# Performance work log

Hardware: AMD Instinct MI355X
Metric: run time of the kernel (lower is better)

Reference implementation:

```python
import jax, jax.numpy as jnp
import numpy as np

# Model dims
C = 16          # in_channels / d_model
D_INNER = 64    # expand * C, expand = 64 // C = 4
HEADDIM = 4
NHEADS = D_INNER // HEADDIM   # 16
D_STATE = 64
D_CONV = 4
CONV_DIM = D_INNER + 2 * D_STATE        # 192 (x, B, C streams)
D_IN_PROJ = 2 * D_INNER + 2 * D_STATE + NHEADS  # 272 (z, xBC, dt)
# Input volume
BSZ, DD, HH, WW = 8, 32, 16, 16
L = DD * HH * WW  # 8192, multiple of 256 -> exact adaptive max pool
POOL = 256


def setup_inputs():
    key = jax.random.key(0)
    ks = jax.random.split(key, 10)
    x = jax.random.normal(ks[0], (BSZ, C, DD, HH, WW), jnp.float32)
    # 3 independent Mamba2 blocks -> stack params with leading dim 3
    Win = jax.random.normal(ks[1], (3, D_IN_PROJ, C), jnp.float32) / np.sqrt(C).astype(np.float32)
    conv_w = jax.random.normal(ks[2], (3, CONV_DIM, D_CONV), jnp.float32) / np.sqrt(D_CONV).astype(np.float32)
    conv_b = jax.random.normal(ks[3], (3, CONV_DIM), jnp.float32) * 0.1
    dt_bias = jax.random.normal(ks[4], (3, NHEADS), jnp.float32) * 0.5
    A_log = jnp.log(jax.random.uniform(ks[5], (3, NHEADS), jnp.float32, minval=1.0, maxval=16.0))
    Dp = jax.random.normal(ks[6], (3, NHEADS), jnp.float32) * 0.5 + 1.0
    norm_w = jnp.ones((3, D_INNER), jnp.float32)
    Wout = jax.random.normal(ks[7], (3, C, D_INNER), jnp.float32) / np.sqrt(D_INNER).astype(np.float32)
    gamma = jnp.ones((3, C), jnp.float32)
    beta = jnp.zeros((3, C), jnp.float32)
    lin_w = jax.random.normal(ks[8], (3, 1, C), jnp.float32) / np.sqrt(C).astype(np.float32)
    lin_b = jnp.zeros((3, 1), jnp.float32)
    return dict(x=x, Win=Win, conv_w=conv_w, conv_b=conv_b, dt_bias=dt_bias,
                A_log=A_log, Dp=Dp, norm_w=norm_w, Wout=Wout,
                gamma=gamma, beta=beta, lin_w=lin_w, lin_b=lin_b)


def _mamba2(u, Win, conv_w, conv_b, dt_bias, A_log, Dp, norm_w, Wout):
    """Mamba2 block: u (B, L, C) -> (B, L, C). ngroups=1, rmsnorm gated."""
    B, Lx, _ = u.shape
    zxbcdt = jnp.einsum('blc,pc->blp', u, Win)  # (B, L, 272)
    z = zxbcdt[..., :D_INNER]
    xBC = zxbcdt[..., D_INNER:D_INNER + CONV_DIM]
    dt = jax.nn.softplus(zxbcdt[..., D_INNER + CONV_DIM:] + dt_bias)  # (B, L, H)
    # causal depthwise conv over time
    conv = jax.lax.conv_general_dilated(
        jnp.transpose(xBC, (0, 2, 1)), conv_w[:, None, :], (1,),
        [(D_CONV - 1, 0)], feature_group_count=CONV_DIM)
    xBC = jax.nn.silu(jnp.transpose(conv, (0, 2, 1)) + conv_b)
    xh = xBC[..., :D_INNER].reshape(B, Lx, NHEADS, HEADDIM)
    Bm = xBC[..., D_INNER:D_INNER + D_STATE]   # (B, L, N)
    Cm = xBC[..., D_INNER + D_STATE:]          # (B, L, N)
    A = -jnp.exp(A_log)                        # (H,)
    dA = jnp.exp(dt * A)                       # (B, L, H)
    dtx = dt[..., None] * xh                   # (B, L, H, P)

    def step(S, inp):
        dA_t, dtx_t, B_t, C_t = inp
        S = S * dA_t[:, :, None, None] + dtx_t[..., None] * B_t[:, None, None, :]
        y_t = jnp.einsum('bhpn,bn->bhp', S, C_t)
        return S, y_t

    S0 = jnp.zeros((B, NHEADS, HEADDIM, D_STATE), u.dtype)
    xs = (jnp.moveaxis(dA, 1, 0), jnp.moveaxis(dtx, 1, 0),
          jnp.moveaxis(Bm, 1, 0), jnp.moveaxis(Cm, 1, 0))
    _, ys = jax.lax.scan(step, S0, xs)                       # (L, B, H, P)
    y = jnp.moveaxis(ys, 0, 1) + Dp[None, None, :, None] * xh
    y = y.reshape(B, Lx, D_INNER) * jax.nn.silu(z)           # gate first
    y = y * jax.lax.rsqrt(jnp.mean(y * y, -1, keepdims=True) + 1e-5) * norm_w
    return jnp.einsum('bld,cd->blc', y, Wout)


def _proj_pool(y, gamma, beta, lw, lb):
    """ReLU -> BatchNorm1d (batch stats) -> Linear(C,1) -> AdaptiveMaxPool1d(256)."""
    B, Lx, _ = y.shape
    v = jax.nn.relu(y.reshape(-1, C))
    mu = jnp.mean(v, 0)
    var = jnp.mean((v - mu) ** 2, 0)
    v = (v - mu) * jax.lax.rsqrt(var + 1e-5) * gamma + beta
    s = (v @ lw.T + lb).reshape(B, Lx)
    return jnp.max(s.reshape(B, POOL, Lx // POOL), -1)  # (B, 256)


def reference(x, Win, conv_w, conv_b, dt_bias, A_log, Dp, norm_w, Wout,
              gamma, beta, lin_w, lin_b):
    B, Cc, Dd, Hh, Ww = x.shape
    Lx = Dd * Hh * Ww
    fD = jnp.transpose(x.reshape(B, Cc, Lx), (0, 2, 1))
    fH = jnp.transpose(jnp.transpose(x, (0, 1, 3, 4, 2)).reshape(B, Cc, Lx), (0, 2, 1))
    fW = jnp.transpose(jnp.transpose(x, (0, 1, 4, 2, 3)).reshape(B, Cc, Lx), (0, 2, 1))
    seqs = jnp.stack([fD, fH, fW], 0)  # (3, B, L, C)
    ys = jax.vmap(_mamba2)(seqs, Win, conv_w, conv_b, dt_bias, A_log, Dp, norm_w, Wout)
    pooled = jax.vmap(_proj_pool)(ys, gamma, beta, lin_w, lin_b)  # (3, B, 256)
    return jnp.concatenate([pooled[0], pooled[1], pooled[2]], -1)[:, None, :]  # (B,1,768)
```

## Files before the change

### kernel.cpp

```cpp
#include <hip/hip_runtime.h>
#include <math.h>

#define CONVD 192
#define NC 128
#define PW 32
#define LOG2E 1.4426950408889634f
#define LN2f  0.69314718055994531f

#define OFF_DST   0u
#define OFF_CHA   4194304u
#define OFF_YS    4210688u
#define OFF_PART  5259264u
#define OFF_TILE  5267456u
#define PD        19947520u

#define TG  0
#define TC  4096
#define TCS 8192
#define TDT 12288
#define TCT 13312

#define XSW(m, t)   ((m) * 64 + (((((t) >> 2) ^ ((m) & 15)) & 15) << 2) + ((t) & 3))
#define XSW4(m, tq) ((m) * 64 + ((((tq) ^ ((m) & 15)) & 15) << 2))

typedef float f32x2 __attribute__((ext_vector_type(2)));

__device__ __forceinline__ f32x2 pk_fma(f32x2 a, f32x2 b, f32x2 c) {
    f32x2 d;
    asm("v_pk_fma_f32 %0, %1, %2, %3" : "=v"(d) : "v"(a), "v"(b), "v"(c));
    return d;
}
__device__ __forceinline__ f32x2 pk_fma_alo(f32x2 a, f32x2 b, f32x2 c) {
    f32x2 d;
    asm("v_pk_fma_f32 %0, %1, %2, %3 op_sel_hi:[0,1,1]" : "=v"(d) : "v"(a), "v"(b), "v"(c));
    return d;
}
__device__ __forceinline__ f32x2 pk_fma_ahi(f32x2 a, f32x2 b, f32x2 c) {
    f32x2 d;
    asm("v_pk_fma_f32 %0, %1, %2, %3 op_sel:[1,0,0]" : "=v"(d) : "v"(a), "v"(b), "v"(c));
    return d;
}
__device__ __forceinline__ f32x2 pk_fma_blo(f32x2 a, f32x2 b, f32x2 c) {
    f32x2 d;
    asm("v_pk_fma_f32 %0, %1, %2, %3 op_sel_hi:[1,0,1]" : "=v"(d) : "v"(a), "v"(b), "v"(c));
    return d;
}
__device__ __forceinline__ f32x2 pk_fma_bhi(f32x2 a, f32x2 b, f32x2 c) {
    f32x2 d;
    asm("v_pk_fma_f32 %0, %1, %2, %3 op_sel:[0,1,0]" : "=v"(d) : "v"(a), "v"(b), "v"(c));
    return d;
}
__device__ __forceinline__ f32x2 lo2(float4 v) { f32x2 r; r.x = v.x; r.y = v.y; return r; }
__device__ __forceinline__ f32x2 hi2(float4 v) { f32x2 r; r.x = v.z; r.y = v.w; return r; }

__device__ __forceinline__ float fast_silu(float x) {
    float e = __builtin_amdgcn_exp2f(-x * LOG2E);
    return x * __builtin_amdgcn_rcpf(1.f + e);
}
__device__ __forceinline__ float fast_softplus(float x) {
    if (x > 20.f) return x;
    float e = __builtin_amdgcn_exp2f(x * LOG2E);
    return LN2f * __builtin_amdgcn_logf(1.f + e);
}

template<int NT, int STRIDE>
__device__ __forceinline__ void stage_u(
    const float* __restrict__ x, float* u_s, int b, int l0, int dir, int tid)
{
    for (int i = tid; i < 67 * 16; i += NT) {
        int pos = i >> 4, c = i & 15;
        int l = l0 + pos - 3;
        float v = 0.f;
        if (l >= 0) {
            if (dir == 0) {
                v = x[(b * 16 + c) * 8192 + l];
            } else if (dir == 1) {
                int h = l >> 9, w = (l >> 5) & 15, d = l & 31;
                v = x[(((b * 16 + c) * 32 + d) * 16 + h) * 16 + w];
            } else {
                int w = l >> 9, d = (l >> 4) & 31, h = l & 15;
                v = x[(((b * 16 + c) * 32 + d) * 16 + h) * 16 + w];
            }
        }
        u_s[pos * STRIDE + c] = v;
    }
}

__device__ __forceinline__ float pk_dot16(const f32x2* u2, const float* wp) {
    float4 w0 = *(const float4*)(wp);
    float4 w1 = *(const float4*)(wp + 4);
    float4 w2 = *(const float4*)(wp + 8);
    float4 w3 = *(const float4*)(wp + 12);
    f32x2 a = {0.f, 0.f};
    a = pk_fma(u2[0], lo2(w0), a);
    a = pk_fma(u2[1], hi2(w0), a);
    a = pk_fma(u2[2], lo2(w1), a);
    a = pk_fma(u2[3], hi2(w1), a);
    a = pk_fma(u2[4], lo2(w2), a);
    a = pk_fma(u2[5], hi2(w2), a);
    a = pk_fma(u2[6], lo2(w3), a);
    a = pk_fma(u2[7], hi2(w3), a);
    return a.x + a.y;
}

__global__ __launch_bounds__(512, 4) void k_delta(
    const float* __restrict__ x, const float* __restrict__ Win,
    const float* __restrict__ convw, const float* __restrict__ convb,
    const float* __restrict__ dtb, const float* __restrict__ A_log,
    float* __restrict__ ws, int dir0, int dslm)
{
    __shared__ float u_s[67 * 17];
    __shared__ float xh_c[4096];
    __shared__ float Bs[4096];
    __shared__ float Cc[4096];
    __shared__ float dts[16 * 65];
    __shared__ float wbuf[16 * 65];
    const int tid = threadIdx.x;
    const int ck = blockIdx.x;
    const int b = blockIdx.y;
    const int dir = dir0 + blockIdx.z;
    float* base = ws + (size_t)(dslm * blockIdx.z) * PD;
    float* Dst = base + OFF_DST;
    float* chA = base + OFF_CHA;
    float* tile = base + OFF_TILE + (size_t)(b * 128 + ck) * 14336;
    const int l0 = ck * 64;
    float* halo = wbuf;

    stage_u<512, 17>(x, u_s, b, l0, dir, tid);
    __syncthreads();

    const int lane = tid & 63;
    const int wv = __builtin_amdgcn_readfirstlane(tid >> 6);

    f32x2 u2[8];
    {
        const float* ur = &u_s[(lane + 3) * 17];
        #pragma unroll
        for (int k = 0; k < 8; k++) { u2[k].x = ur[2 * k]; u2[k].y = ur[2 * k + 1]; }
    }
    if (tid < 192) {
        f32x2 uh2[8];
        #pragma unroll
        for (int pos = 0; pos < 3; pos++) {
            const float* uhr = &u_s[pos * 17];
            #pragma unroll
            for (int k = 0; k < 8; k++) { uh2[k].x = uhr[2 * k]; uh2[k].y = uhr[2 * k + 1]; }
            halo[pos * 192 + tid] = pk_dot16(uh2, Win + (size_t)(dir * 272 + 64 + tid) * 16);
        }
    }
    __syncthreads();

    for (int i = 0; i < 26; i++) {
        const int g = wv * 26 + i;
        const int col = (g < 192) ? (64 + g) : (256 + (g - 192));
        float acc = pk_dot16(u2, Win + (size_t)(dir * 272 + col) * 16);
        if (col < 256) {
            const int ch = col - 64;
            float v1 = __shfl_up(acc, 1);
            float v2 = __shfl_up(acc, 2);
            float v3 = __shfl_up(acc, 3);
            float hh0 = halo[ch];
            float hh1 = halo[192 + ch];
            float hh2 = halo[384 + ch];
            float m1 = (lane >= 1) ? v1 : hh2;
            float m2 = (lane >= 2) ? v2 : ((lane == 0) ? hh1 : hh2);
            float m3 = (lane >= 3) ? v3 : ((lane == 0) ? hh0 : ((lane == 1) ? hh1 : hh2));
            const float* cwp = convw + (size_t)(dir * CONVD + ch) * 4;
            float conv = convb[dir * CONVD + ch]
                       + cwp[0] * m3 + cwp[1] * m2 + cwp[2] * m1 + cwp[3] * acc;
            float xv = fast_silu(conv);
            if (ch < 64)       xh_c[XSW(ch, lane)] = xv;
            else if (ch < 128) Bs[XSW(ch - 64, lane)] = xv;
            else               Cc[XSW(ch - 128, lane)] = xv;
        } else {
            const int h = col - 256;
            float dv = fast_softplus(acc + dtb[dir * 16 + h]);
            dts[h * 65 + lane] = dv;
            tile[TDT + h * 64 + lane] = dv;
        }
    }
    __syncthreads();

    for (int j4 = tid; j4 < 1024; j4 += 512)
        ((float4*)(tile + TC))[j4] = ((const float4*)Cc)[j4];
    for (int h = wv; h < 16; h += 8) {
        float A2 = -expf(A_log[dir * 16 + h]) * LOG2E;
        float dtv = dts[h * 65 + lane];
        float v = dtv * A2;
        #pragma unroll
        for (int off = 1; off < 64; off <<= 1) {
            float o = __shfl_up(v, off, 64);
            if (lane >= off) v += o;
        }
        float tot = __shfl(v, 63, 64);
        tile[TCT + h * 64 + lane] = v;
        wbuf[h * 65 + lane] = __builtin_amdgcn_exp2f(tot - v) * dtv;
        if (lane == 63) chA[(b * 16 + h) * 128 + ck] = __builtin_amdgcn_exp2f(tot);
    }
    __syncthreads();

    for (int j = tid; j < 4096; j += 512) {
        int hp = j >> 6, t = j & 63;
        xh_c[XSW(hp, t)] *= wbuf[(hp >> 2) * 65 + t];
    }
    __syncthreads();

    if (tid < 256) {
        const int hp4 = tid >> 4, n4 = tid & 15;
        f32x2 a2[4][4] = {};
        for (int tq = 0; tq < 16; tq++) {
            float4 xv[4], bv[4];
            #pragma unroll
            for (int i2 = 0; i2 < 4; i2++) {
                xv[i2] = *(const float4*)&xh_c[XSW4(4 * hp4 + i2, tq)];
                bv[i2] = *(const float4*)&Bs[XSW4(4 * n4 + i2, tq)];
            }
            #pragma unroll
            for (int i2 = 0; i2 < 4; i2++)
                #pragma unroll
                for (int j2 = 0; j2 < 4; j2++) {
                    a2[i2][j2] = pk_fma(lo2(xv[i2]), lo2(bv[j2]), a2[i2][j2]);
                    a2[i2][j2] = pk_fma(hi2(xv[i2]), hi2(bv[j2]), a2[i2][j2]);
                }
        }
        #pragma unroll
        for (int i2 = 0; i2 < 4; i2++) {
            int hp = 4 * hp4 + i2;
            int h = hp >> 2, p = hp & 3;
            *(float4*)(Dst + ((size_t)((b * 16 + h) * 128 + ck)) * 256 + p * 64 + 4 * n4) =
                make_float4(a2[i2][0].x + a2[i2][0].y, a2[i2][1].x + a2[i2][1].y,
                            a2[i2][2].x + a2[i2][2].y, a2[i2][3].x + a2[i2][3].y);
        }
    } else {
        const int tg2 = tid - 256;
        const int t4g = tg2 >> 4, x4g = tg2 & 15;
        f32x2 G2[4][2] = {};
        for (int n = 0; n < 64; n++) {
            float4 cr4 = *(const float4*)&Cc[XSW4(n, t4g)];
            float4 br4 = *(const float4*)&Bs[XSW4(n, x4g)];
            f32x2 c01 = lo2(cr4), c23 = hi2(cr4);
            f32x2 b01 = lo2(br4), b23 = hi2(br4);
            G2[0][0] = pk_fma_alo(c01, b01, G2[0][0]); G2[0][1] = pk_fma_alo(c01, b23, G2[0][1]);
            G2[1][0] = pk_fma_ahi(c01, b01, G2[1][0]); G2[1][1] = pk_fma_ahi(c01, b23, G2[1][1]);
            G2[2][0] = pk_fma_alo(c23, b01, G2[2][0]); G2[2][1] = pk_fma_alo(c23, b23, G2[2][1]);
            G2[3][0] = pk_fma_ahi(c23, b01, G2[3][0]); G2[3][1] = pk_fma_ahi(c23, b23, G2[3][1]);
        }
        float* gdst = tile + TG + (size_t)tg2 * 16;
        #pragma unroll
        for (int r = 0; r < 4; r++)
            *(float4*)(gdst + 4 * r) =
                make_float4(G2[r][0].x, G2[r][0].y, G2[r][1].x, G2[r][1].y);
    }
}

__global__ __launch_bounds__(64) void k_chunk_scan(
    float* __restrict__ ws, int dslm)
{
    float* base = ws + (size_t)(dslm * blockIdx.z) * PD;
    float* Dst = base + OFF_DST;
    const float* chA = base + OFF_CHA;
    const int bh = blockIdx.x >> 2;
    const int elem = (blockIdx.x & 3) * 64 + threadIdx.x;
    float S = 0.f;
    for (int k0 = 0; k0 < NC; k0 += 8) {
        float d[8], av[8];
        #pragma unroll
        for (int j = 0; j < 8; j++) {
            d[j] = Dst[((size_t)(bh * 128 + k0 + j)) * 256 + elem];
            av[j] = chA[bh * 128 + k0 + j];
        }
        #pragma unroll
        for (int j = 0; j < 8; j++) {
            Dst[((size_t)(bh * 128 + k0 + j)) * 256 + elem] = S;
            S = av[j] * S + d[j];
        }
    }
}

__global__ __launch_bounds__(256, 4) void k_cs(
    float* __restrict__ ws, int dslm)
{
    __shared__ float Ci[4096];
    __shared__ float SinT[64 * 66];
    float* base = ws + (size_t)(dslm * blockIdx.z) * PD;
    const float* Dst = base + OFF_DST;
    float* tile = base + OFF_TILE + (size_t)(blockIdx.y * 128 + blockIdx.x) * 14336;
    const int tid = threadIdx.x;
    const int b = blockIdx.y;
    const int ck = blockIdx.x;
    const int t4 = tid >> 4, x4 = tid & 15;

    for (int j4 = tid; j4 < 1024; j4 += 256)
        ((float4*)Ci)[j4] = ((const float4*)(tile + TC))[j4];
    for (int j = tid; j < 1024; j += 256) {
        int hp = j >> 4, n4 = (j & 15) << 2;
        int h = hp >> 2, p = hp & 3;
        float4 sv = *(const float4*)(Dst + ((size_t)((b * 16 + h) * 128 + ck)) * 256 + p * 64 + n4);
        SinT[(n4 + 0) * 66 + hp] = sv.x;
        SinT[(n4 + 1) * 66 + hp] = sv.y;
        SinT[(n4 + 2) * 66 + hp] = sv.z;
        SinT[(n4 + 3) * 66 + hp] = sv.w;
    }
    __syncthreads();

    f32x2 C2[4][2] = {};
    for (int n = 0; n < 64; n++) {
        float4 cr4 = *(const float4*)&Ci[XSW4(n, t4)];
        f32x2 c01 = lo2(cr4), c23 = hi2(cr4);
        f32x2 s01 = *(const f32x2*)&SinT[n * 66 + 4 * x4];
        f32x2 s23 = *(const f32x2*)&SinT[n * 66 + 4 * x4 + 2];
        C2[0][0] = pk_fma_alo(c01, s01, C2[0][0]); C2[0][1] = pk_fma_alo(c01, s23, C2[0][1]);
        C2[1][0] = pk_fma_ahi(c01, s01, C2[1][0]); C2[1][1] = pk_fma_ahi(c01, s23, C2[1][1]);
        C2[2][0] = pk_fma_alo(c23, s01, C2[2][0]); C2[2][1] = pk_fma_alo(c23, s23, C2[2][1]);
        C2[3][0] = pk_fma_ahi(c23, s01, C2[3][0]); C2[3][1] = pk_fma_ahi(c23, s23, C2[3][1]);
    }
    float* cdst = tile + TCS + (size_t)tid * 16;
    #pragma unroll
    for (int r = 0; r < 4; r++)
        *(float4*)(cdst + 4 * r) =
            make_float4(C2[r][0].x, C2[r][0].y, C2[r][1].x, C2[r][1].y);
}

__global__ __launch_bounds__(512, 6) void k_out_epi(
    const float* __restrict__ x, const float* __restrict__ Win,
    const float* __restrict__ convw, const float* __restrict__ convb,
    const float* __restrict__ Dp, const float* __restrict__ normw,
    const float* __restrict__ Wout, float* __restrict__ ws, int dir0, int dslm)
{
    __shared__ float uW[67 * 16];
    __shared__ float xh_c[4096];
    __shared__ float zc[4096];
    __shared__ float yv[4096];
    __shared__ float Dps[16];
    __shared__ float red[4][34];
    float* base = ws + (size_t)(dslm * blockIdx.z) * PD;
    float* ys       = base + OFF_YS;
    float* partials = base + OFF_PART;
    const float* tile = base + OFF_TILE + (size_t)(blockIdx.y * 128 + blockIdx.x) * 14336;
    const int dir = dir0 + blockIdx.z;
    const int tid = threadIdx.x;
    const int b = blockIdx.y;
    const int ck = blockIdx.x;
    const int l0 = ck * 64;
    const int tg = tid & 255;
    const int t4 = tg >> 4, x4 = tg & 15;
    const int grp = tid >> 8;
    const int lane = tid & 63;
    const int wv = __builtin_amdgcn_readfirstlane(tid >> 6);
    float* halo = yv;

    stage_u<512, 16>(x, uW, b, l0, dir, tid);
    if (tid < 16) Dps[tid] = Dp[dir * 16 + tid];
    __syncthreads();

    f32x2 u2[8];
    {
        const float* ur = &uW[(lane + 3) * 16];
        #pragma unroll
        for (int k = 0; k < 8; k++) { u2[k].x = ur[2 * k]; u2[k].y = ur[2 * k + 1]; }
    }
    if (tid < 64) {
        f32x2 uh2[8];
        #pragma unroll
        for (int pos = 0; pos < 3; pos++) {
            const float* uhr = &uW[pos * 16];
            #pragma unroll
            for (int k = 0; k < 8; k++) { uh2[k].x = uhr[2 * k]; uh2[k].y = uhr[2 * k + 1]; }
            halo[pos * 64 + tid] = pk_dot16(uh2, Win + (size_t)(dir * 272 + 64 + tid) * 16);
        }
    }
    __syncthreads();

    for (int i = 0; i < 8; i++) {
        const int col = wv * 8 + i;
        zc[XSW(col, lane)] = pk_dot16(u2, Win + (size_t)(dir * 272 + col) * 16);
    }
    for (int i = 0; i < 8; i++) {
        const int ch = wv * 8 + i;
        float acc = pk_dot16(u2, Win + (size_t)(dir * 272 + 64 + ch) * 16);
        float v1 = __shfl_up(acc, 1);
        float v2 = __shfl_up(acc, 2);
        float v3 = __shfl_up(acc, 3);
        float hh0 = halo[ch];
        float hh1 = halo[64 + ch];
        float hh2 = halo[128 + ch];
        float m1 = (lane >= 1) ? v1 : hh2;
        float m2 = (lane >= 2) ? v2 : ((lane == 0) ? hh1 : hh2);
        float m3 = (lane >= 3) ? v3 : ((lane == 0) ? hh0 : ((lane == 1) ? hh1 : hh2));
        const float* cwp = convw + (size_t)(dir * CONVD + ch) * 4;
        float conv = convb[dir * CONVD + ch]
                   + cwp[0] * m3 + cwp[1] * m2 + cwp[2] * m1 + cwp[3] * acc;
        xh_c[XSW(ch, lane)] = fast_silu(conv);
    }
    for (int j = tid; j < 1024; j += 512) {
        int c = j >> 6, d = j & 63;
        uW[c * 65 + d] = Wout[dir * 1024 + j] * normw[dir * 64 + d];
    }
    __syncthreads();

    float G_[4][4];
    {
        const float* gsrc = tile + TG + (size_t)tg * 16;
        #pragma unroll
        for (int r = 0; r < 4; r++) {
            float4 g4 = *(const float4*)(gsrc + 4 * r);
            G_[r][0] = g4.x; G_[r][1] = g4.y; G_[r][2] = g4.z; G_[r][3] = g4.w;
        }
    }

    const int tbase = 4 * t4;
    #pragma unroll 1
    for (int hh = 0; hh < 8; hh++) {
        const int h = 8 * grp + hh;
        const float* ctp = tile + TCT + h * 64;
        const float* dtp = tile + TDT + h * 64;
        float4 ctt4 = *(const float4*)(ctp + tbase);
        const float ctt[4] = {ctt4.x, ctt4.y, ctt4.z, ctt4.w};
        float4 cs4 = *(const float4*)(ctp + 4 * x4);
        float4 dt4 = *(const float4*)(dtp + 4 * x4);
        float4 xq[4];
        #pragma unroll
        for (int p = 0; p < 4; p++) {
            int m = 4 * h + p;
            xq[p] = *(const float4*)&xh_c[m * 64 + (((x4 ^ (m & 15)) & 15) << 2)];
        }
        f32x2 v2[2][4] = {};
        #pragma unroll
        for (int q = 0; q < 4; q++) {
            const int s = 4 * x4 + q;
            float csq = (q == 0) ? cs4.x : (q == 1) ? cs4.y : (q == 2) ? cs4.z : cs4.w;
            float dtq = (q == 0) ? dt4.x : (q == 1) ? dt4.y : (q == 2) ? dt4.z : dt4.w;
            float w[4];
            #pragma unroll
            for (int r = 0; r < 4; r++) {
                float e = __builtin_amdgcn_exp2f(ctt[r] - csq);
                w[r] = (s <= tbase + r) ? (G_[r][q] * dtq) * e : 0.f;
            }
            f32x2 wp0 = {w[0], w[1]};
            f32x2 wp1 = {w[2], w[3]};
            #pragma unroll
            for (int p = 0; p < 4; p++) {
                f32x2 xpair = (q < 2) ? lo2(xq[p]) : hi2(xq[p]);
                if (q & 1) {
                    v2[0][p] = pk_fma_bhi(wp0, xpair, v2[0][p]);
                    v2[1][p] = pk_fma_bhi(wp1, xpair, v2[1][p]);
                } else {
                    v2[0][p] = pk_fma_blo(wp0, xpair, v2[0][p]);
                    v2[1][p] = pk_fma_blo(wp1, xpair, v2[1][p]);
                }
            }
        }
        if (x4 == h) {
            const float* csrc = tile + TCS + (size_t)tg * 16;
            float4 c0 = *(const float4*)(csrc);
            float4 c1 = *(const float4*)(csrc + 4);
            float4 c2 = *(const float4*)(csrc + 8);
            float4 c3 = *(const float4*)(csrc + 12);
            float ect[4];
            #pragma unroll
            for (int r = 0; r < 4; r++) ect[r] = __builtin_amdgcn_exp2f(ctt[r]);
            float cs0[4] = {c0.x, c0.y, c0.z, c0.w};
            float cs1[4] = {c1.x, c1.y, c1.z, c1.w};
            float cs2[4] = {c2.x, c2.y, c2.z, c2.w};
            float cs3[4] = {c3.x, c3.y, c3.z, c3.w};
            #pragma unroll
            for (int p = 0; p < 4; p++) {
                v2[0][p].x += ect[0] * cs0[p];
                v2[0][p].y += ect[1] * cs1[p];
                v2[1][p].x += ect[2] * cs2[p];
                v2[1][p].y += ect[3] * cs3[p];
            }
        }
        float v[16];
        #pragma unroll
        for (int p = 0; p < 4; p++) {
            v[p]      = v2[0][p].x;
            v[4 + p]  = v2[0][p].y;
            v[8 + p]  = v2[1][p].x;
            v[12 + p] = v2[1][p].y;
        }
        #pragma unroll
        for (int j = 0; j < 8; j++) {
            float a = (x4 & 8) ? v[j + 8] : v[j];
            float s_ = (x4 & 8) ? v[j] : v[j + 8];
            v[j] = a + __shfl_xor(s_, 8);
        }
        #pragma unroll
        for (int j = 0; j < 4; j++) {
            float a = (x4 & 4) ? v[j + 4] : v[j];
            float s_ = (x4 & 4) ? v[j] : v[j + 4];
            v[j] = a + __shfl_xor(s_, 4);
        }
        #pragma unroll
        for (int j = 0; j < 2; j++) {
            float a = (x4 & 2) ? v[j + 2] : v[j];
            float s_ = (x4 & 2) ? v[j] : v[j + 2];
            v[j] = a + __shfl_xor(s_, 2);
        }
        {
            float a = (x4 & 1) ? v[1] : v[0];
            float s_ = (x4 & 1) ? v[0] : v[1];
            v[0] = a + __shfl_xor(s_, 1);
        }
        yv[tg * 16 + h] = v[0];
    }
    __syncthreads();

    float os[4];
    const int row = tid >> 2;
    const int p = tid & 3;
    if (tid < 256) {
        float4 ya = *(const float4*)&yv[tid * 16];
        float4 yb = *(const float4*)&yv[tid * 16 + 4];
        float4 yc = *(const float4*)&yv[tid * 16 + 8];
        float4 yd = *(const float4*)&yv[tid * 16 + 12];
        float yval[16] = {ya.x, ya.y, ya.z, ya.w, yb.x, yb.y, yb.z, yb.w,
                          yc.x, yc.y, yc.z, yc.w, yd.x, yd.y, yd.z, yd.w};
        float gg[16], sumsq = 0.f;
        #pragma unroll
        for (int h = 0; h < 16; h++) {
            int m = 4 * h + p;
            int ax = m * 64 + ((((row >> 2) ^ (m & 15)) & 15) << 2) + (row & 3);
            float xh = xh_c[ax];
            float zv = zc[ax];
            float val = (yval[h] + Dps[h] * xh) * fast_silu(zv);
            gg[h] = val;
            sumsq += val * val;
        }
        sumsq += __shfl_xor(sumsq, 1);
        sumsq += __shfl_xor(sumsq, 2);
        float rms = rsqrtf(sumsq * (1.f / 64.f) + 1e-5f);

        float oc[16];
        #pragma unroll
        for (int c = 0; c < 16; c++) {
            float a = 0.f;
            #pragma unroll
            for (int h = 0; h < 16; h++) a += gg[h] * uW[c * 65 + 4 * h + p];
            oc[c] = a;
        }
        #pragma unroll
        for (int c = 0; c < 16; c++) {
            oc[c] += __shfl_xor(oc[c], 1);
            oc[c] += __shfl_xor(oc[c], 2);
        }
        #pragma unroll
        for (int i2 = 0; i2 < 4; i2++) {
            float a0 = (p == 0) ? oc[i2] : oc[4 + i2];
            float a1 = (p == 2) ? oc[8 + i2] : oc[12 + i2];
            os[i2] = (((p & 2) == 0) ? a0 : a1) * rms;
        }
        size_t bl = (size_t)(b * 8192 + l0 + row);
        *(float4*)(ys + bl * 16 + 4 * p) = make_float4(os[0], os[1], os[2], os[3]);

        float bs[4], bq[4];
        #pragma unroll
        for (int i2 = 0; i2 < 4; i2++) {
            float vv = fmaxf(os[i2], 0.f);
            bs[i2] = vv;
            bq[i2] = vv * vv;
        }
        #pragma unroll
        for (int off = 4; off < 64; off <<= 1) {
            #pragma unroll
            for (int i2 = 0; i2 < 4; i2++) {
                bs[i2] += __shfl_xor(bs[i2], off);
                bq[i2] += __shfl_xor(bq[i2], off);
            }
        }
        const int wlane = tid & 63, wvid = tid >> 6;
        if (wlane < 4) {
            #pragma unroll
            for (int i2 = 0; i2 < 4; i2++) {
                red[wvid][4 * wlane + i2] = bs[i2];
                red[wvid][16 + 4 * wlane + i2] = bq[i2];
            }
        }
    }
    __syncthreads();
    if (tid < 32) {
        float a = red[0][tid] + red[1][tid] + red[2][tid] + red[3][tid];
        partials[((size_t)(b * 128 + ck)) * 32 + tid] = a;
    }
}

__global__ __launch_bounds__(256) void k_pool_bn(
    const float* __restrict__ gamma, const float* __restrict__ beta,
    const float* __restrict__ lin_w, const float* __restrict__ lin_b,
    float* __restrict__ ws, float* __restrict__ out, int dir0, int dslm)
{
    float* base = ws + (size_t)(dslm * blockIdx.z) * PD;
    const float* ys = base + OFF_YS;
    const float* partials = base + OFF_PART;
    const int dir = dir0 + blockIdx.z;
    const int tid = threadIdx.x;
    __shared__ float red[8][33];
    __shared__ float cf[18];
    {
        int c = tid & 31, ks = tid >> 5;
        float a = 0.f;
        for (int k = ks * 128; k < ks * 128 + 128; k++) a += partials[k * 32 + c];
        red[ks][c] = a;
    }
    __syncthreads();
    if (tid < 32) {
        float a = 0.f;
        #pragma unroll
        for (int s2 = 1; s2 < 8; s2++) a += red[s2][tid];
        red[0][tid] += a;
    }
    __syncthreads();
    if (tid == 0) {
        float off = lin_b[dir];
        for (int c = 0; c < 16; c++) {
            float mu = red[0][c] * (1.f / 65536.f);
            float var = red[0][16 + c] * (1.f / 65536.f) - mu * mu;
            float inv = rsqrtf(var + 1e-5f);
            float coef = inv * gamma[dir * 16 + c] * lin_w[dir * 16 + c];
            cf[c] = coef;
            off += beta[dir * 16 + c] * lin_w[dir * 16 + c] - mu * coef;
        }
        cf[16] = off;
    }
    __syncthreads();

    const int b = blockIdx.x >> 3;
    const int jg = blockIdx.x & 7;
    const int j = jg * 32 + (tid >> 3);
    const int sub = tid & 7;
    float m = -3.4e38f;
    #pragma unroll
    for (int r = 0; r < 4; r++) {
        int l = j * PW + 8 * r + sub;
        const float* rowp = ys + (size_t)(b * 8192 + l) * 16;
        float sv = cf[16];
        #pragma unroll
        for (int k = 0; k < 4; k++) {
            float4 v4 = *(const float4*)(rowp + 4 * k);
            sv += fmaxf(v4.x, 0.f) * cf[4 * k] + fmaxf(v4.y, 0.f) * cf[4 * k + 1]
                + fmaxf(v4.z, 0.f) * cf[4 * k + 2] + fmaxf(v4.w, 0.f) * cf[4 * k + 3];
        }
        m = fmaxf(m, sv);
    }
    m = fmaxf(m, __shfl_xor(m, 1));
    m = fmaxf(m, __shfl_xor(m, 2));
    m = fmaxf(m, __shfl_xor(m, 4));
    if (sub == 0) out[b * 768 + dir * 256 + j] = m;
}

extern "C" void kernel_launch(void* const* d_in, const int* in_sizes, int n_in,
                              void* d_out, int out_size, void* d_ws, size_t ws_size,
                              hipStream_t stream) {
    const float* x     = (const float*)d_in[0];
    const float* Win   = (const float*)d_in[1];
    const float* convw = (const float*)d_in[2];
    const float* convb = (const float*)d_in[3];
    const float* dtb   = (const float*)d_in[4];
    const float* Alog  = (const float*)d_in[5];
    const float* Dp    = (const float*)d_in[6];
    const float* normw = (const float*)d_in[7];
    const float* Wout  = (const float*)d_in[8];
    const float* gamma = (const float*)d_in[9];
    const float* beta  = (const float*)d_in[10];
    const float* linw  = (const float*)d_in[11];
    const float* linb  = (const float*)d_in[12];
    float* out = (float*)d_out;
    float* ws = (float*)d_ws;

    const bool batched = ws_size >= (size_t)3 * PD * 4;
    const int nz = batched ? 3 : 1;
    const int dslm = batched ? 1 : 0;
    const int nloop = batched ? 1 : 3;

    for (int d0 = 0; d0 < nloop; ++d0) {
        k_delta<<<dim3(128, 8, nz), dim3(512), 0, stream>>>(
            x, Win, convw, convb, dtb, Alog, ws, d0, dslm);
        k_chunk_scan<<<dim3(512, 1, nz), dim3(64), 0, stream>>>(ws, dslm);
        k_cs<<<dim3(128, 8, nz), dim3(256), 0, stream>>>(ws, dslm);
        k_out_epi<<<dim3(128, 8, nz), dim3(512), 0, stream>>>(
            x, Win, convw, convb, Dp, normw, Wout, ws, d0, dslm);
        k_pool_bn<<<dim3(64, 1, nz), dim3(256), 0, stream>>>(
            gamma, beta, linw, linb, ws, out, d0, dslm);
    }
}
```

Measured before the change: 434.1 us.

## Move C-stream projection and C·Bᵀ Gram into chunk-state kernel, recompute instead of staging

New measurement: 364.5 us. 1.19x faster.

```diff
diff --git a/kernel.cpp b/kernel.cpp
--- a/kernel.cpp
+++ b/kernel.cpp
@@ -12,13 +12,12 @@
 #define OFF_YS    4210688u
 #define OFF_PART  5259264u
 #define OFF_TILE  5267456u
-#define PD        19947520u
+#define PD        15753216u
 
 #define TG  0
-#define TC  4096
-#define TCS 8192
-#define TDT 12288
-#define TCT 13312
+#define TCS 4096
+#define TDT 8192
+#define TCT 9216
 
 #define XSW(m, t)   ((m) * 64 + (((((t) >> 2) ^ ((m) & 15)) & 15) << 2) + ((t) & 3))
 #define XSW4(m, tq) ((m) * 64 + ((((tq) ^ ((m) & 15)) & 15) << 2))
@@ -103,7 +102,7 @@
     return a.x + a.y;
 }
 
-__global__ __launch_bounds__(512, 4) void k_delta(
+__global__ __launch_bounds__(512, 6) void k_delta(
     const float* __restrict__ x, const float* __restrict__ Win,
     const float* __restrict__ convw, const float* __restrict__ convb,
     const float* __restrict__ dtb, const float* __restrict__ A_log,
@@ -112,7 +111,6 @@
     __shared__ float u_s[67 * 17];
     __shared__ float xh_c[4096];
     __shared__ float Bs[4096];
-    __shared__ float Cc[4096];
     __shared__ float dts[16 * 65];
     __shared__ float wbuf[16 * 65];
     const int tid = threadIdx.x;
@@ -122,7 +120,7 @@
     float* base = ws + (size_t)(dslm * blockIdx.z) * PD;
     float* Dst = base + OFF_DST;
     float* chA = base + OFF_CHA;
-    float* tile = base + OFF_TILE + (size_t)(b * 128 + ck) * 14336;
+    float* tile = base + OFF_TILE + (size_t)(b * 128 + ck) * 10240;
     const int l0 = ck * 64;
     float* halo = wbuf;
 
@@ -138,21 +136,21 @@
         #pragma unroll
         for (int k = 0; k < 8; k++) { u2[k].x = ur[2 * k]; u2[k].y = ur[2 * k + 1]; }
     }
-    if (tid < 192) {
+    if (tid < 128) {
         f32x2 uh2[8];
         #pragma unroll
         for (int pos = 0; pos < 3; pos++) {
             const float* uhr = &u_s[pos * 17];
             #pragma unroll
             for (int k = 0; k < 8; k++) { uh2[k].x = uhr[2 * k]; uh2[k].y = uhr[2 * k + 1]; }
-            halo[pos * 192 + tid] = pk_dot16(uh2, Win + (size_t)(dir * 272 + 64 + tid) * 16);
-        }
-    }
-    __syncthreads();
-
-    for (int i = 0; i < 26; i++) {
-        const int g = wv * 26 + i;
-        const int col = (g < 192) ? (64 + g) : (256 + (g - 192));
+            halo[pos * 128 + tid] = pk_dot16(uh2, Win + (size_t)(dir * 272 + 64 + tid) * 16);
+        }
+    }
+    __syncthreads();
+
+    for (int i = 0; i < 18; i++) {
+        const int g = wv * 18 + i;
+        const int col = (g < 128) ? (64 + g) : (256 + (g - 128));
         float acc = pk_dot16(u2, Win + (size_t)(dir * 272 + col) * 16);
         if (col < 256) {
             const int ch = col - 64;
@@ -160,8 +158,8 @@
             float v2 = __shfl_up(acc, 2);
             float v3 = __shfl_up(acc, 3);
             float hh0 = halo[ch];
-            float hh1 = halo[192 + ch];
-            float hh2 = halo[384 + ch];
+            float hh1 = halo[128 + ch];
+            float hh2 = halo[256 + ch];
             float m1 = (lane >= 1) ? v1 : hh2;
             float m2 = (lane >= 2) ? v2 : ((lane == 0) ? hh1 : hh2);
             float m3 = (lane >= 3) ? v3 : ((lane == 0) ? hh0 : ((lane == 1) ? hh1 : hh2));
@@ -169,9 +167,8 @@
             float conv = convb[dir * CONVD + ch]
                        + cwp[0] * m3 + cwp[1] * m2 + cwp[2] * m1 + cwp[3] * acc;
             float xv = fast_silu(conv);
-            if (ch < 64)       xh_c[XSW(ch, lane)] = xv;
-            else if (ch < 128) Bs[XSW(ch - 64, lane)] = xv;
-            else               Cc[XSW(ch - 128, lane)] = xv;
+            if (ch < 64) xh_c[XSW(ch, lane)] = xv;
+            else         Bs[XSW(ch - 64, lane)] = xv;
         } else {
             const int h = col - 256;
             float dv = fast_softplus(acc + dtb[dir * 16 + h]);
@@ -181,8 +178,6 @@
     }
     __syncthreads();
 
-    for (int j4 = tid; j4 < 1024; j4 += 512)
-        ((float4*)(tile + TC))[j4] = ((const float4*)Cc)[j4];
     for (int h = wv; h < 16; h += 8) {
         float A2 = -expf(A_log[dir * 16 + h]) * LOG2E;
         float dtv = dts[h * 65 + lane];
@@ -231,25 +226,6 @@
                 make_float4(a2[i2][0].x + a2[i2][0].y, a2[i2][1].x + a2[i2][1].y,
                             a2[i2][2].x + a2[i2][2].y, a2[i2][3].x + a2[i2][3].y);
         }
-    } else {
-        const int tg2 = tid - 256;
-        const int t4g = tg2 >> 4, x4g = tg2 & 15;
-        f32x2 G2[4][2] = {};
-        for (int n = 0; n < 64; n++) {
-            float4 cr4 = *(const float4*)&Cc[XSW4(n, t4g)];
-            float4 br4 = *(const float4*)&Bs[XSW4(n, x4g)];
-            f32x2 c01 = lo2(cr4), c23 = hi2(cr4);
-            f32x2 b01 = lo2(br4), b23 = hi2(br4);
-            G2[0][0] = pk_fma_alo(c01, b01, G2[0][0]); G2[0][1] = pk_fma_alo(c01, b23, G2[0][1]);
-            G2[1][0] = pk_fma_ahi(c01, b01, G2[1][0]); G2[1][1] = pk_fma_ahi(c01, b23, G2[1][1]);
-            G2[2][0] = pk_fma_alo(c23, b01, G2[2][0]); G2[2][1] = pk_fma_alo(c23, b23, G2[2][1]);
-            G2[3][0] = pk_fma_ahi(c23, b01, G2[3][0]); G2[3][1] = pk_fma_ahi(c23, b23, G2[3][1]);
-        }
-        float* gdst = tile + TG + (size_t)tg2 * 16;
-        #pragma unroll
-        for (int r = 0; r < 4; r++)
-            *(float4*)(gdst + 4 * r) =
-                make_float4(G2[r][0].x, G2[r][0].y, G2[r][1].x, G2[r][1].y);
     }
 }
 
@@ -277,22 +253,71 @@
     }
 }
 
-__global__ __launch_bounds__(256, 4) void k_cs(
-    float* __restrict__ ws, int dslm)
+__global__ __launch_bounds__(512, 4) void k_gc(
+    const float* __restrict__ x, const float* __restrict__ Win,
+    const float* __restrict__ convw, const float* __restrict__ convb,
+    float* __restrict__ ws, int dir0, int dslm)
 {
-    __shared__ float Ci[4096];
+    __shared__ float u_s[67 * 17];
+    __shared__ float Bs[4096];
+    __shared__ float Cc[4096];
     __shared__ float SinT[64 * 66];
     float* base = ws + (size_t)(dslm * blockIdx.z) * PD;
     const float* Dst = base + OFF_DST;
-    float* tile = base + OFF_TILE + (size_t)(blockIdx.y * 128 + blockIdx.x) * 14336;
+    float* tile = base + OFF_TILE + (size_t)(blockIdx.y * 128 + blockIdx.x) * 10240;
     const int tid = threadIdx.x;
     const int b = blockIdx.y;
     const int ck = blockIdx.x;
-    const int t4 = tid >> 4, x4 = tid & 15;
-
-    for (int j4 = tid; j4 < 1024; j4 += 256)
-        ((float4*)Ci)[j4] = ((const float4*)(tile + TC))[j4];
-    for (int j = tid; j < 1024; j += 256) {
+    const int l0 = ck * 64;
+    const int lane = tid & 63;
+    const int wv = __builtin_amdgcn_readfirstlane(tid >> 6);
+    float* halo = SinT;
+
+    stage_u<512, 17>(x, u_s, b, l0, dir0 + blockIdx.z, tid);
+    __syncthreads();
+    const int dir = dir0 + blockIdx.z;
+
+    f32x2 u2[8];
+    {
+        const float* ur = &u_s[(lane + 3) * 17];
+        #pragma unroll
+        for (int k = 0; k < 8; k++) { u2[k].x = ur[2 * k]; u2[k].y = ur[2 * k + 1]; }
+    }
+    if (tid < 128) {
+        f32x2 uh2[8];
+        #pragma unroll
+        for (int pos = 0; pos < 3; pos++) {
+            const float* uhr = &u_s[pos * 17];
+            #pragma unroll
+            for (int k = 0; k < 8; k++) { uh2[k].x = uhr[2 * k]; uh2[k].y = uhr[2 * k + 1]; }
+            halo[pos * 128 + tid] = pk_dot16(uh2, Win + (size_t)(dir * 272 + 128 + tid) * 16);
+        }
+    }
+    __syncthreads();
+
+    for (int i = 0; i < 16; i++) {
+        const int col = 128 + wv * 16 + i;
+        const int ch = col - 64;
+        float acc = pk_dot16(u2, Win + (size_t)(dir * 272 + col) * 16);
+        float v1 = __shfl_up(acc, 1);
+        float v2 = __shfl_up(acc, 2);
+        float v3 = __shfl_up(acc, 3);
+        float hh0 = halo[ch - 64];
+        float hh1 = halo[128 + ch - 64];
+        float hh2 = halo[256 + ch - 64];
+        float m1 = (lane >= 1) ? v1 : hh2;
+        float m2 = (lane >= 2) ? v2 : ((lane == 0) ? hh1 : hh2);
+        float m3 = (lane >= 3) ? v3 : ((lane == 0) ? hh0 : ((lane == 1) ? hh1 : hh2));
+        const float* cwp = convw + (size_t)(dir * CONVD + ch) * 4;
+        float conv = convb[dir * CONVD + ch]
+                   + cwp[0] * m3 + cwp[1] * m2 + cwp[2] * m1 + cwp[3] * acc;
+        float xv = fast_silu(conv);
+        if (ch < 128) Bs[XSW(ch - 64, lane)] = xv;
+        else          Cc[XSW(ch - 128, lane)] = xv;
+    }
+    __syncthreads();
+
+    for (int j = tid; j < 1024; j += 512) {
         int hp = j >> 4, n4 = (j & 15) << 2;
         int h = hp >> 2, p = hp & 3;
         float4 sv = *(const float4*)(Dst + ((size_t)((b * 16 + h) * 128 + ck)) * 256 + p * 64 + n4);
@@ -303,22 +328,44 @@
     }
     __syncthreads();
 
-    f32x2 C2[4][2] = {};
-    for (int n = 0; n < 64; n++) {
-        float4 cr4 = *(const float4*)&Ci[XSW4(n, t4)];
-        f32x2 c01 = lo2(cr4), c23 = hi2(cr4);
-        f32x2 s01 = *(const f32x2*)&SinT[n * 66 + 4 * x4];
-        f32x2 s23 = *(const f32x2*)&SinT[n * 66 + 4 * x4 + 2];
-        C2[0][0] = pk_fma_alo(c01, s01, C2[0][0]); C2[0][1] = pk_fma_alo(c01, s23, C2[0][1]);
-        C2[1][0] = pk_fma_ahi(c01, s01, C2[1][0]); C2[1][1] = pk_fma_ahi(c01, s23, C2[1][1]);
-        C2[2][0] = pk_fma_alo(c23, s01, C2[2][0]); C2[2][1] = pk_fma_alo(c23, s23, C2[2][1]);
-        C2[3][0] = pk_fma_ahi(c23, s01, C2[3][0]); C2[3][1] = pk_fma_ahi(c23, s23, C2[3][1]);
-    }
-    float* cdst = tile + TCS + (size_t)tid * 16;
-    #pragma unroll
-    for (int r = 0; r < 4; r++)
-        *(float4*)(cdst + 4 * r) =
-            make_float4(C2[r][0].x, C2[r][0].y, C2[r][1].x, C2[r][1].y);
+    if (tid < 256) {
+        const int t4 = tid >> 4, x4 = tid & 15;
+        f32x2 G2[4][2] = {};
+        for (int n = 0; n < 64; n++) {
+            float4 cr4 = *(const float4*)&Cc[XSW4(n, t4)];
+            float4 br4 = *(const float4*)&Bs[XSW4(n, x4)];
+            f32x2 c01 = lo2(cr4), c23 = hi2(cr4);
+            f32x2 b01 = lo2(br4), b23 = hi2(br4);
+            G2[0][0] = pk_fma_alo(c01, b01, G2[0][0]); G2[0][1] = pk_fma_alo(c01, b23, G2[0][1]);
+            G2[1][0] = pk_fma_ahi(c01, b01, G2[1][0]); G2[1][1] = pk_fma_ahi(c01, b23, G2[1][1]);
+            G2[2][0] = pk_fma_alo(c23, b01, G2[2][0]); G2[2][1] = pk_fma_alo(c23, b23, G2[2][1]);
+            G2[3][0] = pk_fma_ahi(c23, b01, G2[3][0]); G2[3][1] = pk_fma_ahi(c23, b23, G2[3][1]);
+        }
+        float* gdst = tile + TG + (size_t)tid * 16;
+        #pragma unroll
+        for (int r = 0; r < 4; r++)
+            *(float4*)(gdst + 4 * r) =
+                make_float4(G2[r][0].x, G2[r][0].y, G2[r][1].x, G2[r][1].y);
+    } else {
+        const int tg2 = tid - 256;
+        const int t4 = tg2 >> 4, x4 = tg2 & 15;
+        f32x2 C2[4][2] = {};
+        for (int n = 0; n < 64; n++) {
+            float4 cr4 = *(const float4*)&Cc[XSW4(n, t4)];
+            f32x2 c01 = lo2(cr4), c23 = hi2(cr4);
+            f32x2 s01 = *(const f32x2*)&SinT[n * 66 + 4 * x4];
+            f32x2 s23 = *(const f32x2*)&SinT[n * 66 + 4 * x4 + 2];
+            C2[0][0] = pk_fma_alo(c01, s01, C2[0][0]); C2[0][1] = pk_fma_alo(c01, s23, C2[0][1]);
+            C2[1][0] = pk_fma_ahi(c01, s01, C2[1][0]); C2[1][1] = pk_fma_ahi(c01, s23, C2[1][1]);
+            C2[2][0] = pk_fma_alo(c23, s01, C2[2][0]); C2[2][1] = pk_fma_alo(c23, s23, C2[2][1]);
+            C2[3][0] = pk_fma_ahi(c23, s01, C2[3][0]); C2[3][1] = pk_fma_ahi(c23, s23, C2[3][1]);
+        }
+        float* cdst = tile + TCS + (size_t)tg2 * 16;
+        #pragma unroll
+        for (int r = 0; r < 4; r++)
+            *(float4*)(cdst + 4 * r) =
+                make_float4(C2[r][0].x, C2[r][0].y, C2[r][1].x, C2[r][1].y);
+    }
 }
 
 __global__ __launch_bounds__(512, 6) void k_out_epi(
@@ -330,13 +377,13 @@
     __shared__ float uW[67 * 16];
     __shared__ float xh_c[4096];
     __shared__ float zc[4096];
-    __shared__ float yv[4096];
+    __shared__ float yv8[2304];
     __shared__ float Dps[16];
     __shared__ float red[4][34];
     float* base = ws + (size_t)(dslm * blockIdx.z) * PD;
     float* ys       = base + OFF_YS;
     float* partials = base + OFF_PART;
-    const float* tile = base + OFF_TILE + (size_t)(blockIdx.y * 128 + blockIdx.x) * 14336;
+    const float* tile = base + OFF_TILE + (size_t)(blockIdx.y * 128 + blockIdx.x) * 10240;
     const int dir = dir0 + blockIdx.z;
     const int tid = threadIdx.x;
     const int b = blockIdx.y;
@@ -347,7 +394,7 @@
     const int grp = tid >> 8;
     const int lane = tid & 63;
     const int wv = __builtin_amdgcn_readfirstlane(tid >> 6);
-    float* halo = yv;
+    float* halo = yv8;
 
     stage_u<512, 16>(x, uW, b, l0, dir, tid);
     if (tid < 16) Dps[tid] = Dp[dir * 16 + tid];
@@ -408,8 +455,9 @@
         }
     }
 
+    float yreg[8];
     const int tbase = 4 * t4;
-    #pragma unroll 1
+    #pragma unroll
     for (int hh = 0; hh < 8; hh++) {
         const int h = 8 * grp + hh;
         const float* ctp = tile + TCT + h * 64;
@@ -502,7 +550,8 @@
             float s_ = (x4 & 1) ? v[0] : v[1];
             v[0] = a + __shfl_xor(s_, 1);
         }
-        yv[tg * 16 + h] = v[0];
+        if (grp) yv8[tg * 9 + hh] = v[0];
+        else     yreg[hh] = v[0];
     }
     __syncthreads();
 
@@ -510,12 +559,12 @@
     const int row = tid >> 2;
     const int p = tid & 3;
     if (tid < 256) {
-        float4 ya = *(const float4*)&yv[tid * 16];
-        float4 yb = *(const float4*)&yv[tid * 16 + 4];
-        float4 yc = *(const float4*)&yv[tid * 16 + 8];
-        float4 yd = *(const float4*)&yv[tid * 16 + 12];
-        float yval[16] = {ya.x, ya.y, ya.z, ya.w, yb.x, yb.y, yb.z, yb.w,
-                          yc.x, yc.y, yc.z, yc.w, yd.x, yd.y, yd.z, yd.w};
+        float yval[16];
+        #pragma unroll
+        for (int hh = 0; hh < 8; hh++) {
+            yval[hh] = yreg[hh];
+            yval[8 + hh] = yv8[tid * 9 + hh];
+        }
         float gg[16], sumsq = 0.f;
         #pragma unroll
         for (int h = 0; h < 16; h++) {
@@ -676,7 +725,8 @@
         k_delta<<<dim3(128, 8, nz), dim3(512), 0, stream>>>(
             x, Win, convw, convb, dtb, Alog, ws, d0, dslm);
         k_chunk_scan<<<dim3(512, 1, nz), dim3(64), 0, stream>>>(ws, dslm);
-        k_cs<<<dim3(128, 8, nz), dim3(256), 0, stream>>>(ws, dslm);
+        k_gc<<<dim3(128, 8, nz), dim3(512), 0, stream>>>(
+            x, Win, convw, convb, ws, d0, dslm);
         k_out_epi<<<dim3(128, 8, nz), dim3(512), 0, stream>>>(
             x, Win, convw, convb, Dp, normw, Wout, ws, d0, dslm);
         k_pool_bn<<<dim3(64, 1, nz), dim3(256), 0, stream>>>(
```
